# Performance work log

Measured on AMD Instinct MI355X. Metric: run time of the kernel, lower is better.

The kernel has to match this reference:

```python
import jax, jax.numpy as jnp
from jax import lax
import numpy as np

B, T, D_IN, H = 4096, 64, 300, 3


def setup_inputs() -> dict:
    key = jax.random.key(0)
    k_x, k_len, k_wih, k_whh, k_bih, k_bhh = jax.random.split(key, 6)
    x = jax.random.normal(k_x, (B, T, D_IN), dtype=jnp.float32)
    lengths = jax.random.randint(k_len, (B,), 1, T + 1, dtype=jnp.int64)
    # PyTorch nn.RNN init: uniform(-1/sqrt(H), 1/sqrt(H))
    bound = 1.0 / np.sqrt(H)
    W_ih = jax.random.uniform(k_wih, (H, D_IN), jnp.float32, -bound, bound)
    W_hh = jax.random.uniform(k_whh, (H, H), jnp.float32, -bound, bound)
    b_ih = jax.random.uniform(k_bih, (H,), jnp.float32, -bound, bound)
    b_hh = jax.random.uniform(k_bhh, (H,), jnp.float32, -bound, bound)
    return {"x": x, "lengths": lengths, "W_ih": W_ih, "W_hh": W_hh,
            "b_ih": b_ih, "b_hh": b_hh}


def reference(x, lengths, W_ih, W_hh, b_ih, b_hh):
    # Tanh RNN over packed variable-length sequences. The packed RNN returns
    # hidden = h at step lengths[i]-1 for each sample i; we emulate packing
    # with a masked scan: h only updates while t < lengths[i].
    Bn, Tn, _ = x.shape
    # Hoist the input projection into one big GEMM: [B,T,H]
    xb = jnp.einsum('bti,hi->bth', x, W_ih) + b_ih
    mask = jnp.arange(Tn)[None, :] < lengths[:, None]  # [B,T] bool

    def step(h, inp):
        xt, m = inp  # xt: [B,H], m: [B,1]
        h_new = jnp.tanh(xt + h @ W_hh.T + b_hh)
        return jnp.where(m, h_new, h), None

    h0 = jnp.zeros((Bn, W_hh.shape[0]), dtype=x.dtype)
    h_last, _ = lax.scan(step, h0,
                         (xb.transpose(1, 0, 2), mask.T[:, :, None]))
    return h_last  # [B, H] == hidden.squeeze(0)
```

## Files before the change

kernel.cpp:

```cpp
#include <hip/hip_runtime.h>
#include <math.h>

#define B_ 4096
#define T_ 64
#define DIN_ 300
#define H_ 3
#define NF4 75

#define XB_OFF 65536

__global__ void prep_lengths_kernel(const int* __restrict__ lraw,
                                    int* __restrict__ len32, int B) {
  __shared__ int flag;
  if (threadIdx.x == 0) flag = 0;
  __syncthreads();
  int local = 0;
  int half = B >> 1;
  for (int i = threadIdx.x; i < half; i += blockDim.x)
    if (lraw[2 * i + 1] != 0) local = 1;
  if (local) atomicOr(&flag, 1);
  __syncthreads();
  int is32 = flag;
  for (int i = threadIdx.x; i < B; i += blockDim.x) {
    int v = is32 ? lraw[i] : lraw[2 * i];
    if (v < 1) v = 1;
    if (v > T_) v = T_;
    len32[i] = v;
  }
}

__global__ __launch_bounds__(256) void proj_kernel(
    const float* __restrict__ x,
    const int* __restrict__ len,
    const float* __restrict__ W_ih,
    float* __restrict__ xb) {
  const int b = blockIdx.x;
  const int tid = threadIdx.x;

  __shared__ float4 Wl[H_][76];
  if (tid < H_ * NF4) {
    int h = tid / NF4;
    int i = tid - h * NF4;
    Wl[h][i] = reinterpret_cast<const float4*>(W_ih)[h * NF4 + i];
  }
  const int L = len[b];
  __syncthreads();

  const int wave = tid >> 6;
  const int lane = tid & 63;
  const int g = lane >> 2;
  const int s = lane & 3;
  const int row = wave * 16 + g;
  if (wave * 16 >= L) return;

  const bool rowok = (row < L);
  const float4* xr = reinterpret_cast<const float4*>(
      x + (size_t)b * (T_ * DIN_) + (size_t)row * DIN_);

  float a0 = 0.f, a1 = 0.f, a2 = 0.f;
#pragma unroll 4
  for (int k = 0; k < 19; ++k) {
    int idx = 4 * k + s;
    if (rowok && idx < NF4) {
      float4 v = xr[idx];
      float4 w0 = Wl[0][idx];
      float4 w1 = Wl[1][idx];
      float4 w2 = Wl[2][idx];
      a0 += v.x * w0.x + v.y * w0.y + v.z * w0.z + v.w * w0.w;
      a1 += v.x * w1.x + v.y * w1.y + v.z * w1.z + v.w * w1.w;
      a2 += v.x * w2.x + v.y * w2.y + v.z * w2.z + v.w * w2.w;
    }
  }
  a0 += __shfl_xor(a0, 1);
  a1 += __shfl_xor(a1, 1);
  a2 += __shfl_xor(a2, 1);
  a0 += __shfl_xor(a0, 2);
  a1 += __shfl_xor(a1, 2);
  a2 += __shfl_xor(a2, 2);

  if (s == 0 && rowok) {
    float* o = xb + ((size_t)row * B_ + b) * H_;
    o[0] = a0;
    o[1] = a1;
    o[2] = a2;
  }
}

__device__ __forceinline__ float fast_tanh(float x) {
  float xc = fminf(fmaxf(x, -9.0f), 9.0f);
  float t = __expf(2.0f * xc);
  return (t - 1.0f) * __builtin_amdgcn_rcpf(t + 1.0f);
}

__global__ __launch_bounds__(256) void tail_kernel(
    const int* __restrict__ len, const float* __restrict__ xb,
    const float* __restrict__ W_hh, const float* __restrict__ b_ih,
    const float* __restrict__ b_hh, float* __restrict__ out) {
  const int b = blockIdx.x * blockDim.x + threadIdx.x;
  if (b >= B_) return;
  const float w00 = W_hh[0], w01 = W_hh[1], w02 = W_hh[2];
  const float w10 = W_hh[3], w11 = W_hh[4], w12 = W_hh[5];
  const float w20 = W_hh[6], w21 = W_hh[7], w22 = W_hh[8];
  const float c0 = b_ih[0] + b_hh[0];
  const float c1 = b_ih[1] + b_hh[1];
  const float c2 = b_ih[2] + b_hh[2];
  const int L = len[b];
  float h0 = 0.f, h1 = 0.f, h2 = 0.f;
  const float* p = xb + (size_t)b * H_;
  for (int t = 0; t < L; ++t) {
    const float* q = p + (size_t)t * (B_ * H_);
    float a0 = q[0] + c0 + w00 * h0 + w01 * h1 + w02 * h2;
    float a1 = q[1] + c1 + w10 * h0 + w11 * h1 + w12 * h2;
    float a2 = q[2] + c2 + w20 * h0 + w21 * h1 + w22 * h2;
    h0 = fast_tanh(a0);
    h1 = fast_tanh(a1);
    h2 = fast_tanh(a2);
  }
  out[b * 3 + 0] = h0;
  out[b * 3 + 1] = h1;
  out[b * 3 + 2] = h2;
}

extern "C" void kernel_launch(void* const* d_in, const int* in_sizes, int n_in,
                              void* d_out, int out_size, void* d_ws,
                              size_t ws_size, hipStream_t stream) {
  const float* x = (const float*)d_in[0];
  const int* lraw = (const int*)d_in[1];
  const float* W_ih = (const float*)d_in[2];
  const float* W_hh = (const float*)d_in[3];
  const float* b_ih = (const float*)d_in[4];
  const float* b_hh = (const float*)d_in[5];
  float* out = (float*)d_out;

  int* len32 = (int*)d_ws;
  float* xb = (float*)((char*)d_ws + XB_OFF);

  prep_lengths_kernel<<<1, 256, 0, stream>>>(lraw, len32, B_);
  proj_kernel<<<B_, 256, 0, stream>>>(x, len32, W_ih, xb);
  tail_kernel<<<(B_ + 255) / 256, 256, 0, stream>>>(len32, xb, W_hh, b_ih,
                                                    b_hh, out);
}
```

Baseline: 440.0 us.

## Fuse length prep, input projection and recurrence into one kernel

Merges the three kernels into a single per-sample block. Lengths are decoded inline by checking lraw[1], and the projected inputs stay in shared memory, where thread 0 runs the 3-wide recurrence. This removes two launches and the global round trip for xb. In exchange, the serial recurrence now runs on one thread per block while the other threads sit idle. The int64 check is also weaker: it looks only at element 1, where the old kernel scanned every high word.

```diff
diff --git a/kernel.cpp b/kernel.cpp
--- a/kernel.cpp
+++ b/kernel.cpp
@@ -7,43 +7,36 @@
 #define H_ 3
 #define NF4 75
 
-#define XB_OFF 65536
-
-__global__ void prep_lengths_kernel(const int* __restrict__ lraw,
-                                    int* __restrict__ len32, int B) {
-  __shared__ int flag;
-  if (threadIdx.x == 0) flag = 0;
-  __syncthreads();
-  int local = 0;
-  int half = B >> 1;
-  for (int i = threadIdx.x; i < half; i += blockDim.x)
-    if (lraw[2 * i + 1] != 0) local = 1;
-  if (local) atomicOr(&flag, 1);
-  __syncthreads();
-  int is32 = flag;
-  for (int i = threadIdx.x; i < B; i += blockDim.x) {
-    int v = is32 ? lraw[i] : lraw[2 * i];
-    if (v < 1) v = 1;
-    if (v > T_) v = T_;
-    len32[i] = v;
-  }
+__device__ __forceinline__ float fast_tanh(float x) {
+  float xc = fminf(fmaxf(x, -9.0f), 9.0f);
+  float t = __expf(2.0f * xc);
+  return (t - 1.0f) * __builtin_amdgcn_rcpf(t + 1.0f);
 }
 
-__global__ __launch_bounds__(256) void proj_kernel(
+__global__ __launch_bounds__(256) void rnn_fused_kernel(
     const float* __restrict__ x,
-    const int* __restrict__ len,
+    const int* __restrict__ lraw,
     const float* __restrict__ W_ih,
-    float* __restrict__ xb) {
+    const float* __restrict__ W_hh,
+    const float* __restrict__ b_ih,
+    const float* __restrict__ b_hh,
+    float* __restrict__ out) {
   const int b = blockIdx.x;
   const int tid = threadIdx.x;
 
   __shared__ float4 Wl[H_][76];
+  __shared__ float4 xb_s[T_];
+
   if (tid < H_ * NF4) {
     int h = tid / NF4;
     int i = tid - h * NF4;
     Wl[h][i] = reinterpret_cast<const float4*>(W_ih)[h * NF4 + i];
   }
-  const int L = len[b];
+
+  const bool is32 = (lraw[1] != 0);
+  int L = is32 ? lraw[b] : lraw[2 * b];
+  if (L < 1) L = 1;
+  if (L > T_) L = T_;
   __syncthreads();
 
   const int wave = tid >> 6;
@@ -51,70 +44,55 @@
   const int g = lane >> 2;
   const int s = lane & 3;
   const int row = wave * 16 + g;
-  if (wave * 16 >= L) return;
 
-  const bool rowok = (row < L);
-  const float4* xr = reinterpret_cast<const float4*>(
-      x + (size_t)b * (T_ * DIN_) + (size_t)row * DIN_);
+  if (wave * 16 < L) {
+    const bool rowok = (row < L);
+    const float4* xr = reinterpret_cast<const float4*>(
+        x + (size_t)b * (T_ * DIN_) + (size_t)row * DIN_);
 
-  float a0 = 0.f, a1 = 0.f, a2 = 0.f;
+    float a0 = 0.f, a1 = 0.f, a2 = 0.f;
 #pragma unroll 4
-  for (int k = 0; k < 19; ++k) {
-    int idx = 4 * k + s;
-    if (rowok && idx < NF4) {
-      float4 v = xr[idx];
-      float4 w0 = Wl[0][idx];
-      float4 w1 = Wl[1][idx];
-      float4 w2 = Wl[2][idx];
-      a0 += v.x * w0.x + v.y * w0.y + v.z * w0.z + v.w * w0.w;
-      a1 += v.x * w1.x + v.y * w1.y + v.z * w1.z + v.w * w1.w;
-      a2 += v.x * w2.x + v.y * w2.y + v.z * w2.z + v.w * w2.w;
+    for (int k = 0; k < 19; ++k) {
+      int idx = 4 * k + s;
+      if (rowok && idx < NF4) {
+        float4 v = xr[idx];
+        float4 w0 = Wl[0][idx];
+        float4 w1 = Wl[1][idx];
+        float4 w2 = Wl[2][idx];
+        a0 += v.x * w0.x + v.y * w0.y + v.z * w0.z + v.w * w0.w;
+        a1 += v.x * w1.x + v.y * w1.y + v.z * w1.z + v.w * w1.w;
+        a2 += v.x * w2.x + v.y * w2.y + v.z * w2.z + v.w * w2.w;
+      }
     }
+    a0 += __shfl_xor(a0, 1);
+    a1 += __shfl_xor(a1, 1);
+    a2 += __shfl_xor(a2, 1);
+    a0 += __shfl_xor(a0, 2);
+    a1 += __shfl_xor(a1, 2);
+    a2 += __shfl_xor(a2, 2);
+    if (s == 0 && rowok) xb_s[row] = make_float4(a0, a1, a2, 0.f);
   }
-  a0 += __shfl_xor(a0, 1);
-  a1 += __shfl_xor(a1, 1);
-  a2 += __shfl_xor(a2, 1);
-  a0 += __shfl_xor(a0, 2);
-  a1 += __shfl_xor(a1, 2);
-  a2 += __shfl_xor(a2, 2);
+  __syncthreads();
 
-  if (s == 0 && rowok) {
-    float* o = xb + ((size_t)row * B_ + b) * H_;
-    o[0] = a0;
-    o[1] = a1;
-    o[2] = a2;
-  }
-}
+  if (tid != 0) return;
 
-__device__ __forceinline__ float fast_tanh(float x) {
-  float xc = fminf(fmaxf(x, -9.0f), 9.0f);
-  float t = __expf(2.0f * xc);
-  return (t - 1.0f) * __builtin_amdgcn_rcpf(t + 1.0f);
-}
-
-__global__ __launch_bounds__(256) void tail_kernel(
-    const int* __restrict__ len, const float* __restrict__ xb,
-    const float* __restrict__ W_hh, const float* __restrict__ b_ih,
-    const float* __restrict__ b_hh, float* __restrict__ out) {
-  const int b = blockIdx.x * blockDim.x + threadIdx.x;
-  if (b >= B_) return;
   const float w00 = W_hh[0], w01 = W_hh[1], w02 = W_hh[2];
   const float w10 = W_hh[3], w11 = W_hh[4], w12 = W_hh[5];
   const float w20 = W_hh[6], w21 = W_hh[7], w22 = W_hh[8];
   const float c0 = b_ih[0] + b_hh[0];
   const float c1 = b_ih[1] + b_hh[1];
   const float c2 = b_ih[2] + b_hh[2];
-  const int L = len[b];
   float h0 = 0.f, h1 = 0.f, h2 = 0.f;
-  const float* p = xb + (size_t)b * H_;
+  float4 cur = xb_s[0];
   for (int t = 0; t < L; ++t) {
-    const float* q = p + (size_t)t * (B_ * H_);
-    float a0 = q[0] + c0 + w00 * h0 + w01 * h1 + w02 * h2;
-    float a1 = q[1] + c1 + w10 * h0 + w11 * h1 + w12 * h2;
-    float a2 = q[2] + c2 + w20 * h0 + w21 * h1 + w22 * h2;
+    float4 nxt = xb_s[(t + 1 < L) ? t + 1 : t];
+    float a0 = cur.x + c0 + w00 * h0 + w01 * h1 + w02 * h2;
+    float a1 = cur.y + c1 + w10 * h0 + w11 * h1 + w12 * h2;
+    float a2 = cur.z + c2 + w20 * h0 + w21 * h1 + w22 * h2;
     h0 = fast_tanh(a0);
     h1 = fast_tanh(a1);
     h2 = fast_tanh(a2);
+    cur = nxt;
   }
   out[b * 3 + 0] = h0;
   out[b * 3 + 1] = h1;
@@ -132,11 +110,6 @@
   const float* b_hh = (const float*)d_in[5];
   float* out = (float*)d_out;
 
-  int* len32 = (int*)d_ws;
-  float* xb = (float*)((char*)d_ws + XB_OFF);
-
-  prep_lengths_kernel<<<1, 256, 0, stream>>>(lraw, len32, B_);
-  proj_kernel<<<B_, 256, 0, stream>>>(x, len32, W_ih, xb);
-  tail_kernel<<<(B_ + 255) / 256, 256, 0, stream>>>(len32, xb, W_hh, b_ih,
-                                                    b_hh, out);
+  rnn_fused_kernel<<<B_, 256, 0, stream>>>(x, lraw, W_ih, W_hh, b_ih, b_hh,
+                                           out);
 }
```

New measurement: 414.2 us. 1.06x faster.
